# Performance work log

Hardware: AMD Instinct MI355X
Metric: run time of the kernel (lower is better)

Reference implementation:

```python
import jax, jax.numpy as jnp
import numpy as np

NHEAD = 8
K_NEIGH = 16


def setup_inputs() -> dict:
    key = jax.random.key(0)
    ks = jax.random.split(key, 6)
    B, L, D = 4, 4096, 512
    x = jax.random.normal(ks[0], (B, L, D), dtype=jnp.float32)
    positions = jax.random.uniform(ks[1], (B, L, 3), dtype=jnp.float32)
    in_proj_w = jax.random.normal(ks[2], (3 * D, D), dtype=jnp.float32) * 0.02
    in_proj_b = jax.random.normal(ks[3], (3 * D,), dtype=jnp.float32) * 0.02
    out_proj_w = jax.random.normal(ks[4], (D, D), dtype=jnp.float32) * 0.02
    out_proj_b = jax.random.normal(ks[5], (D,), dtype=jnp.float32) * 0.02
    return {"x": x, "positions": positions, "in_proj_w": in_proj_w,
            "in_proj_b": in_proj_b, "out_proj_w": out_proj_w, "out_proj_b": out_proj_b}


def _sparse_attention(x, positions, in_proj_w, in_proj_b, out_proj_w, out_proj_b):
    B, L, D = x.shape
    H, dh = NHEAD, D // NHEAD
    K = min(K_NEIGH, L)
    scale = 1.0 / jnp.sqrt(jnp.asarray(dh, x.dtype))

    # Pairwise distances [B, L, L]; topk smallest -> neighbor indices [B, L, K].
    diff = positions[:, :, None, :] - positions[:, None, :, :]
    dist = jnp.sqrt(jnp.sum(diff * diff, axis=-1))
    _, nbr = jax.lax.top_k(-dist, K)  # [B, L, K]

    Wq, Wk, Wv = in_proj_w[:D], in_proj_w[D:2 * D], in_proj_w[2 * D:]
    bq, bk, bv = in_proj_b[:D], in_proj_b[D:2 * D], in_proj_b[2 * D:]

    # Query is x[b, i] itself (self is always its own nearest neighbor at dist 0),
    # so the selected attention row equals attention with query x[b, i] over neighbors.
    q = ((x @ Wq.T + bq) * scale).reshape(B, L, H, dh)

    # Gather neighbor features: [B, L, K, D]
    b_idx = jnp.arange(B)[:, None, None]
    local_x = x[b_idx, nbr]
    k = (local_x @ Wk.T + bk).reshape(B, L, K, H, dh)
    v = (local_x @ Wv.T + bv).reshape(B, L, K, H, dh)

    scores = jnp.einsum('blhd,blkhd->blhk', q, k)
    attn = jax.nn.softmax(scores, axis=-1)
    ctx = jnp.einsum('blhk,blkhd->blhd', attn, v).reshape(B, L, D)
    out = ctx @ out_proj_w.T + out_proj_b

    # Faithful fallback: if i not among its neighbors, pass through x[b, i].
    is_in = jnp.any(nbr == jnp.arange(L)[None, :, None], axis=-1)  # [B, L]
    return jnp.where(is_in[..., None], out, x)


def reference(x, positions, in_proj_w, in_proj_b, out_proj_w, out_proj_b):
    return _sparse_attention(x, positions, in_proj_w, in_proj_b, out_proj_w, out_proj_b)
```

## Files before the change

kernel.cpp:

```cpp
#include <hip/hip_runtime.h>
#include <cfloat>
#include <cmath>

constexpr int B = 4;
constexpr int L = 4096;
constexpr int D = 512;
constexpr int NH = 8;
constexpr int DH = 64;
constexpr int KN = 16;
constexpr int M = B * L;
constexpr int N_IN = 3 * D;
constexpr int NCELL = 512;

typedef __attribute__((ext_vector_type(8))) short short8;
typedef __attribute__((ext_vector_type(4))) float f32x4;
typedef unsigned short ushort;

__device__ __forceinline__ ushort f2bf(float f) {
  unsigned u = __float_as_uint(f);
  u = u + 0x7fffu + ((u >> 16) & 1u);
  return (ushort)(u >> 16);
}
__device__ __forceinline__ float bf2f(ushort h) {
  return __uint_as_float(((unsigned)h) << 16);
}
__device__ __forceinline__ float dot8(const uint4 qu, const uint4 ku, float a) {
  a = fmaf(bf2f((ushort)qu.x), bf2f((ushort)ku.x), a);
  a = fmaf(bf2f((ushort)(qu.x >> 16)), bf2f((ushort)(ku.x >> 16)), a);
  a = fmaf(bf2f((ushort)qu.y), bf2f((ushort)ku.y), a);
  a = fmaf(bf2f((ushort)(qu.y >> 16)), bf2f((ushort)(ku.y >> 16)), a);
  a = fmaf(bf2f((ushort)qu.z), bf2f((ushort)ku.z), a);
  a = fmaf(bf2f((ushort)(qu.z >> 16)), bf2f((ushort)(ku.z >> 16)), a);
  a = fmaf(bf2f((ushort)qu.w), bf2f((ushort)ku.w), a);
  a = fmaf(bf2f((ushort)(qu.w >> 16)), bf2f((ushort)(ku.w >> 16)), a);
  return a;
}
__device__ __forceinline__ void acc8(float wgt, const uint4 vv, float (&acc)[8]) {
  acc[0] = fmaf(wgt, bf2f((ushort)vv.x), acc[0]);
  acc[1] = fmaf(wgt, bf2f((ushort)(vv.x >> 16)), acc[1]);
  acc[2] = fmaf(wgt, bf2f((ushort)vv.y), acc[2]);
  acc[3] = fmaf(wgt, bf2f((ushort)(vv.y >> 16)), acc[3]);
  acc[4] = fmaf(wgt, bf2f((ushort)vv.z), acc[4]);
  acc[5] = fmaf(wgt, bf2f((ushort)(vv.z >> 16)), acc[5]);
  acc[6] = fmaf(wgt, bf2f((ushort)vv.w), acc[6]);
  acc[7] = fmaf(wgt, bf2f((ushort)(vv.w >> 16)), acc[7]);
}
__device__ __forceinline__ uint2 pack4hi(const float4 v) {
  uint2 o;
  o.x = (unsigned)f2bf(v.x) | ((unsigned)f2bf(v.y) << 16);
  o.y = (unsigned)f2bf(v.z) | ((unsigned)f2bf(v.w) << 16);
  return o;
}
__device__ __forceinline__ void gload16(const void* g, void* l) {
  __builtin_amdgcn_global_load_lds(
      (const __attribute__((address_space(1))) void*)g,
      (__attribute__((address_space(3))) void*)l, 16, 0, 0);
}
__device__ __forceinline__ int morton3(int x, int y, int z) {
  int m = 0;
#pragma unroll
  for (int i = 0; i < 3; ++i)
    m |= (((x >> i) & 1) << (3 * i + 2)) | (((y >> i) & 1) << (3 * i + 1)) |
         (((z >> i) & 1) << (3 * i));
  return m;
}

__global__ __launch_bounds__(256) void cvt_x_kernel(const float* __restrict__ in,
                                                    ushort* __restrict__ out) {
  const int n8 = M * D / 8;
  for (int i = blockIdx.x * 256 + threadIdx.x; i < n8; i += gridDim.x * 256) {
    const float4 v0 = reinterpret_cast<const float4*>(in)[i * 2];
    const float4 v1 = reinterpret_cast<const float4*>(in)[i * 2 + 1];
    uint4 o;
    const uint2 a = pack4hi(v0), b2 = pack4hi(v1);
    o.x = a.x; o.y = a.y; o.z = b2.x; o.w = b2.y;
    reinterpret_cast<uint4*>(out)[i] = o;
  }
}

__global__ __launch_bounds__(256) void cvt_w_kernel(const float* __restrict__ in_w,
                                                    const float* __restrict__ out_w,
                                                    ushort* __restrict__ iwh,
                                                    ushort* __restrict__ owh,
                                                    ushort* __restrict__ owl) {
  const int ni8 = N_IN * D / 8;
  const int no8 = D * D / 8;
  for (int i = blockIdx.x * 256 + threadIdx.x; i < ni8 + no8; i += gridDim.x * 256) {
    if (i < ni8) {
      const float4 v0 = reinterpret_cast<const float4*>(in_w)[i * 2];
      const float4 v1 = reinterpret_cast<const float4*>(in_w)[i * 2 + 1];
      uint4 o;
      const uint2 a = pack4hi(v0), b2 = pack4hi(v1);
      o.x = a.x; o.y = a.y; o.z = b2.x; o.w = b2.y;
      reinterpret_cast<uint4*>(iwh)[i] = o;
    } else {
      const int j = i - ni8;
      const float4 v0 = reinterpret_cast<const float4*>(out_w)[j * 2];
      const float4 v1 = reinterpret_cast<const float4*>(out_w)[j * 2 + 1];
      uint4 oh, ol;
      const uint2 a = pack4hi(v0), b2 = pack4hi(v1);
      oh.x = a.x; oh.y = a.y; oh.z = b2.x; oh.w = b2.y;
      const float4 r0 = make_float4(v0.x - bf2f(f2bf(v0.x)), v0.y - bf2f(f2bf(v0.y)),
                                    v0.z - bf2f(f2bf(v0.z)), v0.w - bf2f(f2bf(v0.w)));
      const float4 r1 = make_float4(v1.x - bf2f(f2bf(v1.x)), v1.y - bf2f(f2bf(v1.y)),
                                    v1.z - bf2f(f2bf(v1.z)), v1.w - bf2f(f2bf(v1.w)));
      const uint2 c = pack4hi(r0), d2 = pack4hi(r1);
      ol.x = c.x; ol.y = c.y; ol.z = d2.x; ol.w = d2.y;
      reinterpret_cast<uint4*>(owh)[j] = oh;
      reinterpret_cast<uint4*>(owl)[j] = ol;
    }
  }
}

__global__ __launch_bounds__(512) void sort_kernel(const float* __restrict__ pos,
                                                   int* __restrict__ qorder) {
  __shared__ int hist[NCELL];
  __shared__ int scanbuf[NCELL];
  const int b = blockIdx.x;
  const int t = threadIdx.x;
  hist[t] = 0;
  __syncthreads();

  int cells[8], ranks[8];
  const float* p = pos + (size_t)b * L * 3;
#pragma unroll
  for (int q = 0; q < 8; ++q) {
    const int i = q * 512 + t;
    const int ix = min(7, max(0, (int)(p[3 * i + 0] * 8.f)));
    const int iy = min(7, max(0, (int)(p[3 * i + 1] * 8.f)));
    const int iz = min(7, max(0, (int)(p[3 * i + 2] * 8.f)));
    cells[q] = morton3(ix, iy, iz);
    ranks[q] = atomicAdd(&hist[cells[q]], 1);
  }
  __syncthreads();

  int accv = hist[t];
  const int orig = accv;
  scanbuf[t] = accv;
  __syncthreads();
  for (int s = 1; s < NCELL; s <<= 1) {
    const int o = (t >= s) ? scanbuf[t - s] : 0;
    __syncthreads();
    accv += o;
    scanbuf[t] = accv;
    __syncthreads();
  }
  hist[t] = accv - orig;
  __syncthreads();

#pragma unroll
  for (int q = 0; q < 8; ++q) {
    const int i = q * 512 + t;
    qorder[b * L + hist[cells[q]] + ranks[q]] = i;
  }
}

constexpr int TP = 65;

__global__ __launch_bounds__(512) void topk_kernel(const float* __restrict__ pos,
                                                   int* __restrict__ nbr,
                                                   int* __restrict__ isin) {
  __shared__ float sxT[64 * TP], syT[64 * TP], szT[64 * TP];
  __shared__ unsigned long long lst[8 * 64];
  const int wave = threadIdx.x >> 6;
  const int lane = threadIdx.x & 63;
  const int b = blockIdx.x >> 9;
  const int l = (blockIdx.x & 511) * 8 + wave;
  const int row = b * L + l;

  const float* p = pos + (size_t)b * L * 3;
  for (int i = threadIdx.x; i < L; i += 512) {
    const int a = (i & 63) * TP + (i >> 6);
    sxT[a] = p[3 * i + 0];
    syT[a] = p[3 * i + 1];
    szT[a] = p[3 * i + 2];
  }
  __syncthreads();

  const int qa = (l & 63) * TP + (l >> 6);
  const float qx = sxT[qa], qy = syT[qa], qz = szT[qa];

  float mA = FLT_MAX, mB2 = FLT_MAX, mC = FLT_MAX, mD2 = FLT_MAX;
  const int base = lane * TP;
  for (int j = 0; j < 64; j += 4) {
#define D2(t, acc)                                                   \
    {                                                                \
      const int a = base + j + t;                                    \
      const float dx = qx - sxT[a], dy = qy - syT[a], dz = qz - szT[a]; \
      acc = fminf(acc, fmaf(dx, dx, fmaf(dy, dy, dz * dz)));         \
    }
    D2(0, mA) D2(1, mB2) D2(2, mC) D2(3, mD2)
#undef D2
  }
  const unsigned mbits = __float_as_uint(fminf(fminf(mA, mB2), fminf(mC, mD2)));

  unsigned lo = 1, hi = 0x40400001u;
  while (lo < hi) {
    const unsigned mid = (lo + hi) >> 1;
    const int c = __popcll(__ballot(mbits < mid));
    if (c >= 16) hi = mid; else lo = mid + 1;
  }
  const unsigned P = lo + 16;

  int cnt = 0;
  unsigned long long am = __ballot(mbits < P);
  const unsigned long long below = (1ull << lane) - 1ull;
  while (am) {
    const int pl = (int)__builtin_ctzll(am);
    am &= am - 1;
    const int a = pl * TP + lane;
    const float dx = qx - sxT[a], dy = qy - syT[a], dz = qz - szT[a];
    const float d2 = fmaf(dx, dx, fmaf(dy, dy, dz * dz));
    const bool hit = __float_as_uint(d2) < P;
    const unsigned long long msk = __ballot(hit);
    if (hit) {
      const int slot = cnt + __popcll(msk & below);
      if (slot < 64) {
        const unsigned c = (unsigned)(lane * 64 + pl);
        lst[wave * 64 + slot] =
            ((unsigned long long)__float_as_uint(sqrtf(d2)) << 32) | c;
      }
    }
    cnt += __popcll(msk);
  }
  const int n = min(cnt, 64);

  const unsigned long long mine = (lane < n) ? lst[wave * 64 + lane] : ~0ull;
  int r = 0;
  for (int i = 0; i < n; ++i) r += (lst[wave * 64 + i] < mine) ? 1 : 0;

  const int idx = (int)(unsigned)(mine & 0xffffffffu);
  const bool wr = (lane < n) && (r < 16);
  if (wr) nbr[(size_t)row * KN + r] = idx;
  const unsigned long long hit2 = __ballot(wr && idx == l);
  if (lane == 0) isin[row] = hit2 ? 1 : 0;
}

constexpr int BM = 128, BN = 128, BK = 32;

__global__ __launch_bounds__(256) void gemm_in(const ushort* __restrict__ A,
                                               const ushort* __restrict__ W,
                                               const float* __restrict__ bias,
                                               ushort* __restrict__ qb,
                                               ushort* __restrict__ kb,
                                               ushort* __restrict__ vb) {
  __shared__ ushort Ah[BM * BK];
  __shared__ ushort Bh[BN * BK];

  const int tid = threadIdx.x;
  const int m0 = blockIdx.x * BM;
  const int n0 = blockIdx.y * BN;

  const int wv = tid >> 6;
  const int lane = tid & 63;
  const int sr = wv * 16 + (lane >> 2);
  const int sc = (lane & 3) * 8;
  const ushort* Asrc = A + (size_t)(m0 + sr) * D + sc;
  const ushort* Wsrc = W + (size_t)(n0 + sr) * D + sc;
  ushort* AhB0 = Ah + (wv * 16) * BK;
  ushort* AhB1 = Ah + (wv * 16 + 64) * BK;
  ushort* BhB0 = Bh + (wv * 16) * BK;
  ushort* BhB1 = Bh + (wv * 16 + 64) * BK;

  const int wr0 = (wv >> 1) * 64;
  const int wc0 = (wv & 1) * 64;
  const int fr_row = lane & 15;
  const int kof = (lane >> 4) * 8;

  f32x4 acc[4][4];
#pragma unroll
  for (int i = 0; i < 4; ++i)
#pragma unroll
    for (int j = 0; j < 4; ++j) acc[i][j] = {0.f, 0.f, 0.f, 0.f};

  for (int k0 = 0; k0 < D; k0 += BK) {
    __syncthreads();
    gload16(Asrc + k0, AhB0);
    gload16(Asrc + (size_t)64 * D + k0, AhB1);
    gload16(Wsrc + k0, BhB0);
    gload16(Wsrc + (size_t)64 * D + k0, BhB1);
    __syncthreads();

    short8 ah[4];
#pragma unroll
    for (int fr = 0; fr < 4; ++fr)
      ah[fr] = *reinterpret_cast<const short8*>(&Ah[(wr0 + fr * 16 + fr_row) * BK + kof]);
#pragma unroll
    for (int fc = 0; fc < 4; ++fc) {
      const short8 bh = *reinterpret_cast<const short8*>(&Bh[(wc0 + fc * 16 + fr_row) * BK + kof]);
#pragma unroll
      for (int fr = 0; fr < 4; ++fr)
        acc[fr][fc] = __builtin_amdgcn_mfma_f32_16x16x32_bf16(ah[fr], bh, acc[fr][fc], 0, 0, 0);
    }
  }

  const int region = n0 >> 9;
  ushort* outb = region == 0 ? qb : (region == 1 ? kb : vb);
  const float scl = region == 0 ? 0.125f : 1.0f;
  const int nloc0 = (n0 & 511) + wc0;
#pragma unroll
  for (int fr = 0; fr < 4; ++fr) {
#pragma unroll
    for (int r = 0; r < 4; ++r) {
      const int grow = m0 + wr0 + fr * 16 + (lane >> 4) * 4 + r;
#pragma unroll
      for (int fc = 0; fc < 4; ++fc) {
        const int cc = fc * 16 + (lane & 15);
        const float v = (acc[fr][fc][r] + bias[n0 + wc0 + cc]) * scl;
        outb[(size_t)grow * D + nloc0 + cc] = f2bf(v);
      }
    }
  }
}

__global__ __launch_bounds__(256) void gemm_out(const ushort* __restrict__ A,
                                                const ushort* __restrict__ Wh,
                                                const ushort* __restrict__ Wl,
                                                const float* __restrict__ bias,
                                                float* __restrict__ C,
                                                const float* __restrict__ X,
                                                const int* __restrict__ isin) {
  __shared__ ushort Ah[BM * BK];
  __shared__ ushort Bh[BN * BK];
  __shared__ ushort Bl[BN * BK];

  const int tid = threadIdx.x;
  const int m0 = blockIdx.x * BM;
  const int n0 = blockIdx.y * BN;

  const int wv = tid >> 6;
  const int lane = tid & 63;
  const int sr = wv * 16 + (lane >> 2);
  const int sc = (lane & 3) * 8;
  const ushort* Asrc = A + (size_t)(m0 + sr) * D + sc;
  const ushort* Hsrc = Wh + (size_t)(n0 + sr) * D + sc;
  const ushort* Lsrc = Wl + (size_t)(n0 + sr) * D + sc;
  ushort* AhB0 = Ah + (wv * 16) * BK;
  ushort* AhB1 = Ah + (wv * 16 + 64) * BK;
  ushort* BhB0 = Bh + (wv * 16) * BK;
  ushort* BhB1 = Bh + (wv * 16 + 64) * BK;
  ushort* BlB0 = Bl + (wv * 16) * BK;
  ushort* BlB1 = Bl + (wv * 16 + 64) * BK;

  const int wr0 = (wv >> 1) * 64;
  const int wc0 = (wv & 1) * 64;
  const int fr_row = lane & 15;
  const int kof = (lane >> 4) * 8;

  f32x4 acc[4][4];
#pragma unroll
  for (int i = 0; i < 4; ++i)
#pragma unroll
    for (int j = 0; j < 4; ++j) acc[i][j] = {0.f, 0.f, 0.f, 0.f};

  for (int k0 = 0; k0 < D; k0 += BK) {
    __syncthreads();
    gload16(Asrc + k0, AhB0);
    gload16(Asrc + (size_t)64 * D + k0, AhB1);
    gload16(Hsrc + k0, BhB0);
    gload16(Hsrc + (size_t)64 * D + k0, BhB1);
    gload16(Lsrc + k0, BlB0);
    gload16(Lsrc + (size_t)64 * D + k0, BlB1);
    __syncthreads();

    short8 ah[4];
#pragma unroll
    for (int fr = 0; fr < 4; ++fr)
      ah[fr] = *reinterpret_cast<const short8*>(&Ah[(wr0 + fr * 16 + fr_row) * BK + kof]);
#pragma unroll
    for (int fc = 0; fc < 4; ++fc) {
      const short8 bh = *reinterpret_cast<const short8*>(&Bh[(wc0 + fc * 16 + fr_row) * BK + kof]);
      const short8 bl = *reinterpret_cast<const short8*>(&Bl[(wc0 + fc * 16 + fr_row) * BK + kof]);
#pragma unroll
      for (int fr = 0; fr < 4; ++fr) {
        acc[fr][fc] = __builtin_amdgcn_mfma_f32_16x16x32_bf16(ah[fr], bh, acc[fr][fc], 0, 0, 0);
        acc[fr][fc] = __builtin_amdgcn_mfma_f32_16x16x32_bf16(ah[fr], bl, acc[fr][fc], 0, 0, 0);
      }
    }
  }

#pragma unroll
  for (int fr = 0; fr < 4; ++fr) {
#pragma unroll
    for (int r = 0; r < 4; ++r) {
      const int grow = m0 + wr0 + fr * 16 + (lane >> 4) * 4 + r;
      const int ok = isin[grow];
#pragma unroll
      for (int fc = 0; fc < 4; ++fc) {
        const int gcol = n0 + wc0 + fc * 16 + (lane & 15);
        float v = acc[fr][fc][r] + bias[gcol];
        if (!ok) v = X[(size_t)grow * D + gcol];
        C[(size_t)grow * D + gcol] = v;
      }
    }
  }
}

__global__ __launch_bounds__(256) void attn_kernel(const ushort* __restrict__ qb,
                                                   const ushort* __restrict__ kb,
                                                   const ushort* __restrict__ vb,
                                                   const int* __restrict__ nbr,
                                                   const int* __restrict__ qorder,
                                                   ushort* __restrict__ ctx) {
  const int wave = threadIdx.x >> 6;
  const int lane = threadIdx.x & 63;
  const int xcd = blockIdx.x & 7;
  const int chunk = blockIdx.x >> 3;
  const int b = xcd >> 1;
  const int slot = ((xcd & 1) * 512 + chunk) * 4 + wave;
  const int l = qorder[b * L + slot];
  const int bl = b * L + l;
  const int bbase = b * L;
  const int* nb = nbr + (size_t)bl * KN;

  const int h = lane >> 3;
  const int n0 = lane & 7;
  const int glane = h * 8;

  const ushort* qp = qb + (size_t)bl * D + h * DH;
  uint4 qv[8];
#pragma unroll
  for (int i = 0; i < 8; ++i)
    qv[i] = *reinterpret_cast<const uint4*>(qp + i * 8);

  const int j0 = nb[n0];
  const int j1 = nb[n0 + 8];
  float a0 = 0.f, a1 = 0.f;
  {
    const ushort* kr0 = kb + (size_t)(bbase + j0) * D + h * DH;
    const ushort* kr1 = kb + (size_t)(bbase + j1) * D + h * DH;
#pragma unroll
    for (int i = 0; i < 8; ++i) {
      a0 = dot8(qv[i], *reinterpret_cast<const uint4*>(kr0 + i * 8), a0);
      a1 = dot8(qv[i], *reinterpret_cast<const uint4*>(kr1 + i * 8), a1);
    }
  }

  float mx = fmaxf(a0, a1);
  mx = fmaxf(mx, __shfl_xor(mx, 1));
  mx = fmaxf(mx, __shfl_xor(mx, 2));
  mx = fmaxf(mx, __shfl_xor(mx, 4));
  const float e0 = expf(a0 - mx), e1 = expf(a1 - mx);
  float sm = e0 + e1;
  sm += __shfl_xor(sm, 1);
  sm += __shfl_xor(sm, 2);
  sm += __shfl_xor(sm, 4);
  const float inv = 1.0f / sm;
  const float w0 = e0 * inv, w1 = e1 * inv;

  float ww[KN];
  int jj[KN];
#pragma unroll
  for (int n = 0; n < KN; ++n) {
    const int src = glane + (n & 7);
    ww[n] = __shfl((n < 8) ? w0 : w1, src);
    jj[n] = __shfl((n < 8) ? j0 : j1, src);
  }

  const int d0 = n0 * 8;
  const ushort* vbase = vb + (size_t)bbase * D + h * DH + d0;
  float acc[8];
#pragma unroll
  for (int i = 0; i < 8; ++i) acc[i] = 0.f;

#pragma unroll
  for (int g = 0; g < KN; g += 4) {
    const uint4 va0 = *reinterpret_cast<const uint4*>(vbase + (size_t)jj[g] * D);
    const uint4 va1 = *reinterpret_cast<const uint4*>(vbase + (size_t)jj[g + 1] * D);
    const uint4 va2 = *reinterpret_cast<const uint4*>(vbase + (size_t)jj[g + 2] * D);
    const uint4 va3 = *reinterpret_cast<const uint4*>(vbase + (size_t)jj[g + 3] * D);
    acc8(ww[g], va0, acc);
    acc8(ww[g + 1], va1, acc);
    acc8(ww[g + 2], va2, acc);
    acc8(ww[g + 3], va3, acc);
  }

  uint4 o;
  o.x = (unsigned)f2bf(acc[0]) | ((unsigned)f2bf(acc[1]) << 16);
  o.y = (unsigned)f2bf(acc[2]) | ((unsigned)f2bf(acc[3]) << 16);
  o.z = (unsigned)f2bf(acc[4]) | ((unsigned)f2bf(acc[5]) << 16);
  o.w = (unsigned)f2bf(acc[6]) | ((unsigned)f2bf(acc[7]) << 16);
  *reinterpret_cast<uint4*>(ctx + (size_t)bl * D + h * DH + d0) = o;
}

extern "C" void kernel_launch(void* const* d_in, const int* in_sizes, int n_in,
                              void* d_out, int out_size, void* d_ws, size_t ws_size,
                              hipStream_t stream) {
  const float* x     = (const float*)d_in[0];
  const float* pos   = (const float*)d_in[1];
  const float* in_w  = (const float*)d_in[2];
  const float* in_b  = (const float*)d_in[3];
  const float* out_w = (const float*)d_in[4];
  const float* out_b = (const float*)d_in[5];
  float* out = (float*)d_out;

  const size_t nbr_bytes  = (size_t)M * KN * sizeof(int);
  const size_t isin_bytes = (size_t)M * sizeof(int);
  const size_t half_bytes = (size_t)M * D * sizeof(ushort);
  const size_t iwh_bytes  = (size_t)N_IN * D * sizeof(ushort);
  const size_t ow_bytes   = (size_t)D * D * sizeof(ushort);
  const size_t sort_bytes = (size_t)M * sizeof(int);
  const size_t need = nbr_bytes + isin_bytes + 5 * half_bytes +
                      iwh_bytes + 2 * ow_bytes + sort_bytes + 16384;
  if (ws_size < need) return;

  char* w = (char*)d_ws;
  int*    nbr    = (int*)w;    w += (nbr_bytes + 255) & ~(size_t)255;
  int*    isin   = (int*)w;    w += (isin_bytes + 255) & ~(size_t)255;
  ushort* xb     = (ushort*)w; w += (half_bytes + 255) & ~(size_t)255;
  ushort* qb     = (ushort*)w; w += (half_bytes + 255) & ~(size_t)255;
  ushort* kb     = (ushort*)w; w += (half_bytes + 255) & ~(size_t)255;
  ushort* vb     = (ushort*)w; w += (half_bytes + 255) & ~(size_t)255;
  ushort* ctxb   = (ushort*)w; w += (half_bytes + 255) & ~(size_t)255;
  ushort* iwh    = (ushort*)w; w += (iwh_bytes + 255) & ~(size_t)255;
  ushort* owh    = (ushort*)w; w += (ow_bytes + 255) & ~(size_t)255;
  ushort* owl    = (ushort*)w; w += (ow_bytes + 255) & ~(size_t)255;
  int*    qorder = (int*)w;

  cvt_x_kernel<<<2048, 256, 0, stream>>>(x, xb);
  cvt_w_kernel<<<512, 256, 0, stream>>>(in_w, out_w, iwh, owh, owl);

  sort_kernel<<<B, 512, 0, stream>>>(pos, qorder);

  topk_kernel<<<B * (L / 8), 512, 0, stream>>>(pos, nbr, isin);

  gemm_in<<<dim3(M / BM, N_IN / BN), 256, 0, stream>>>(xb, iwh, in_b, qb, kb, vb);

  attn_kernel<<<M / 4, 256, 0, stream>>>(qb, kb, vb, nbr, qorder, ctxb);

  gemm_out<<<dim3(M / BM, D / BN), 256, 0, stream>>>(ctxb, owh, owl, out_b, out, x, isin);
}
```

Before: 172.7 us.

## Double GEMM K-tile to 64 and XOR-swizzle LDS layout in input projection

The QKV input-projection GEMM now stages 64-wide K slices instead of 32, which halves the number of barrier pairs per tile. The shared-memory layout applies an XOR swizzle of 16-byte chunks by row, so global-to-LDS loads and MFMA fragment reads avoid bank conflicts. This doubles LDS use per block, which may reduce occupancy.

```diff
diff --git a/kernel.cpp b/kernel.cpp
--- a/kernel.cpp
+++ b/kernel.cpp
@@ -237,6 +237,7 @@
 }
 
 constexpr int BM = 128, BN = 128, BK = 32;
+constexpr int BK2 = 64;
 
 __global__ __launch_bounds__(256) void gemm_in(const ushort* __restrict__ A,
                                                const ushort* __restrict__ W,
@@ -244,8 +245,8 @@
                                                ushort* __restrict__ qb,
                                                ushort* __restrict__ kb,
                                                ushort* __restrict__ vb) {
-  __shared__ ushort Ah[BM * BK];
-  __shared__ ushort Bh[BN * BK];
+  __shared__ ushort Ah[BM * BK2];
+  __shared__ ushort Bh[BN * BK2];
 
   const int tid = threadIdx.x;
   const int m0 = blockIdx.x * BM;
@@ -253,19 +254,24 @@
 
   const int wv = tid >> 6;
   const int lane = tid & 63;
-  const int sr = wv * 16 + (lane >> 2);
-  const int sc = (lane & 3) * 8;
-  const ushort* Asrc = A + (size_t)(m0 + sr) * D + sc;
-  const ushort* Wsrc = W + (size_t)(n0 + sr) * D + sc;
-  ushort* AhB0 = Ah + (wv * 16) * BK;
-  ushort* AhB1 = Ah + (wv * 16 + 64) * BK;
-  ushort* BhB0 = Bh + (wv * 16) * BK;
-  ushort* BhB1 = Bh + (wv * 16 + 64) * BK;
+  const int srow0 = wv * 8 + (lane >> 3);
+  const int gchunk = (lane & 7) ^ (lane >> 3);
+  const ushort* Asrc = A + (size_t)(m0 + srow0) * D + gchunk * 8;
+  const ushort* Wsrc = W + (size_t)(n0 + srow0) * D + gchunk * 8;
+  ushort* AhB0 = Ah + (wv * 8) * BK2;
+  ushort* AhB1 = Ah + (wv * 8 + 32) * BK2;
+  ushort* AhB2 = Ah + (wv * 8 + 64) * BK2;
+  ushort* AhB3 = Ah + (wv * 8 + 96) * BK2;
+  ushort* BhB0 = Bh + (wv * 8) * BK2;
+  ushort* BhB1 = Bh + (wv * 8 + 32) * BK2;
+  ushort* BhB2 = Bh + (wv * 8 + 64) * BK2;
+  ushort* BhB3 = Bh + (wv * 8 + 96) * BK2;
 
   const int wr0 = (wv >> 1) * 64;
   const int wc0 = (wv & 1) * 64;
   const int fr_row = lane & 15;
-  const int kof = (lane >> 4) * 8;
+  const int cbase = lane >> 4;
+  const int rx = lane & 7;
 
   f32x4 acc[4][4];
 #pragma unroll
@@ -273,24 +279,34 @@
 #pragma unroll
     for (int j = 0; j < 4; ++j) acc[i][j] = {0.f, 0.f, 0.f, 0.f};
 
-  for (int k0 = 0; k0 < D; k0 += BK) {
+  for (int k0 = 0; k0 < D; k0 += BK2) {
     __syncthreads();
     gload16(Asrc + k0, AhB0);
-    gload16(Asrc + (size_t)64 * D + k0, AhB1);
+    gload16(Asrc + (size_t)32 * D + k0, AhB1);
+    gload16(Asrc + (size_t)64 * D + k0, AhB2);
+    gload16(Asrc + (size_t)96 * D + k0, AhB3);
     gload16(Wsrc + k0, BhB0);
-    gload16(Wsrc + (size_t)64 * D + k0, BhB1);
+    gload16(Wsrc + (size_t)32 * D + k0, BhB1);
+    gload16(Wsrc + (size_t)64 * D + k0, BhB2);
+    gload16(Wsrc + (size_t)96 * D + k0, BhB3);
     __syncthreads();
 
-    short8 ah[4];
-#pragma unroll
-    for (int fr = 0; fr < 4; ++fr)
-      ah[fr] = *reinterpret_cast<const short8*>(&Ah[(wr0 + fr * 16 + fr_row) * BK + kof]);
-#pragma unroll
-    for (int fc = 0; fc < 4; ++fc) {
-      const short8 bh = *reinterpret_cast<const short8*>(&Bh[(wc0 + fc * 16 + fr_row) * BK + kof]);
+#pragma unroll
+    for (int kk = 0; kk < 2; ++kk) {
+      const int slot = (kk * 4 + cbase) ^ rx;
+      short8 ah[4];
 #pragma unroll
       for (int fr = 0; fr < 4; ++fr)
-        acc[fr][fc] = __builtin_amdgcn_mfma_f32_16x16x32_bf16(ah[fr], bh, acc[fr][fc], 0, 0, 0);
+        ah[fr] = *reinterpret_cast<const short8*>(
+            &Ah[(wr0 + fr * 16 + fr_row) * BK2 + slot * 8]);
+#pragma unroll
+      for (int fc = 0; fc < 4; ++fc) {
+        const short8 bh = *reinterpret_cast<const short8*>(
+            &Bh[(wc0 + fc * 16 + fr_row) * BK2 + slot * 8]);
+#pragma unroll
+        for (int fr = 0; fr < 4; ++fr)
+          acc[fr][fc] = __builtin_amdgcn_mfma_f32_16x16x32_bf16(ah[fr], bh, acc[fr][fc], 0, 0, 0);
+      }
     }
   }
 
```

Result: faster. 166.3 us (-3.7%).
